# Performance work log

Measured on AMD Instinct MI355X. Metric: run time of the kernel, lower is better.

The kernel has to match this reference:

```python
import jax, jax.numpy as jnp
import numpy as np


def setup_inputs() -> dict:
    key = jax.random.key(0)
    ks = jax.random.split(key, 5)
    S, B, D, H, CTX = 2, 1024, 128, 512, 128
    W_SCALE = 0.05
    return {
        "context": jax.random.normal(ks[0], (B, CTX), dtype=jnp.float32),
        "eps": jax.random.normal(ks[1], (S, B, D), dtype=jnp.float32),
        "W1": jax.random.normal(ks[2], (H, D), dtype=jnp.float32) * W_SCALE,
        "Wc": jax.random.normal(ks[3], (H, CTX), dtype=jnp.float32) * W_SCALE,
        "b1": jnp.zeros((H,), dtype=jnp.float32),
        "W2": jax.random.normal(ks[4], (2 * D, H), dtype=jnp.float32) * W_SCALE,
        "b2": jnp.zeros((2 * D,), dtype=jnp.float32),
    }


def _made_masks(D, H, dtype):
    # standard MADE natural-ordering masks, 1 hidden layer, 2 output params per dim
    m_in = jnp.arange(1, D + 1)                      # input degrees 1..D
    m_h = (jnp.arange(H) % (D - 1)) + 1              # hidden degrees 1..D-1
    M1 = (m_h[:, None] >= m_in[None, :]).astype(dtype)   # (H, D)
    m_out = jnp.tile(m_in, 2)                        # (2D,) mean then pre_scale
    M2 = (m_out[:, None] > m_h[None, :]).astype(dtype)   # (2D, H)
    return M1, M2


def reference(context, eps, W1, Wc, b1, W2, b2):
    # for d in range(D): full MADE forward, take column d of (mu, scale),
    # z[:, d] = mu_d + softplus(pre_scale_d) * eps_d  (reparameterized Normal sample)
    S, B, D = eps.shape
    H = W1.shape[0]
    M1, M2 = _made_masks(D, H, W1.dtype)
    W1m = W1 * M1            # (H, D)
    W2m = W2 * M2            # (2D, H)
    ctx_term = context @ Wc.T + b1   # (B, H), shared across S samples

    def made(z):             # z: (S, B, D) -> (S, B, 2D)
        h = jax.nn.relu(jnp.einsum('sbd,hd->sbh', z, W1m) + ctx_term)
        return jnp.einsum('sbh,oh->sbo', h, W2m) + b2

    def step(z, xs):
        d, eps_d = xs        # d: scalar int, eps_d: (S, B)
        out = made(z)        # full re-forward each dim, as in the torch loop
        mu_d = jnp.take(out, d, axis=-1)             # (S, B)
        pre_scale_d = jnp.take(out, d + D, axis=-1)  # (S, B)
        scale_d = jax.nn.softplus(pre_scale_d)
        z_d = mu_d + scale_d * eps_d                 # Normal(mu, scale).rsample()
        z = z.at[:, :, d].set(z_d)                   # index_put on column d
        return z, None

    z0 = jnp.zeros_like(eps)
    xs = (jnp.arange(D), jnp.moveaxis(eps, -1, 0))   # per-step noise (D, S, B)
    z_samples, _ = jax.lax.scan(step, z0, xs)
    return z_samples
```

## Files before the change

### kernel.cpp

```cpp
#include <hip/hip_runtime.h>
#include <math.h>

constexpr int S_   = 2;
constexpr int B_   = 1024;
constexpr int D_   = 128;
constexpr int H_   = 512;
constexpr int CTX_ = 128;

__device__ __forceinline__ int h_of_u(int u) {
    return (u < 508) ? ((u >> 2) + 127 * (u & 3)) : u;
}
__device__ __forceinline__ int g_of_u(int u) {
    return (u < 508) ? ((u >> 2) + 1) : (u - 507);
}
__device__ __forceinline__ float rlaneF(float v, int l) {
    return __int_as_float(__builtin_amdgcn_readlane(__float_as_int(v), l));
}
__device__ __forceinline__ float softplus_fast(float x) {
    return __logf(1.f + __expf(x));
}

typedef unsigned int  uint32x4 __attribute__((ext_vector_type(4)));
typedef unsigned int  uint32x2 __attribute__((ext_vector_type(2)));
typedef _Float16      half8    __attribute__((ext_vector_type(8)));
typedef _Float16      half4v   __attribute__((ext_vector_type(4)));
typedef _Float16      half2v   __attribute__((ext_vector_type(2)));
typedef __fp16        fp16x2   __attribute__((ext_vector_type(2)));
union U16 { uint32x4 u; half8 h; half2v h2[4]; };
union U8  { uint32x2 u; half4v h; };
union H2U { half2v h; fp16x2 f; unsigned int u; };
union FU  { uint32x4 u; float4 f; };

#if __has_builtin(__builtin_amdgcn_fdot2)
__device__ __forceinline__ float fdot2f(half2v a, half2v b, float c) {
    return __builtin_amdgcn_fdot2(a, b, c, false);
}
#else
__device__ __forceinline__ float fdot2f(half2v a, half2v b, float c) {
    return fmaf((float)a[0], (float)b[0], fmaf((float)a[1], (float)b[1], c));
}
#endif
#if __has_builtin(__builtin_amdgcn_cvt_pkrtz)
__device__ __forceinline__ half2v pk2(float a, float b) {
    H2U t; t.f = __builtin_amdgcn_cvt_pkrtz(a, b);
    return t.h;
}
#else
__device__ __forceinline__ half2v pk2(float a, float b) {
    half2v r; r[0] = (_Float16)a; r[1] = (_Float16)b; return r;
}
#endif

constexpr int N_WT = 16 * 2048;
constexpr size_t WS_WT_OFF   = 0;
constexpr size_t WS_W0_OFF   = (size_t)N_WT * 16;
constexpr size_t WS_WPX_OFF  = WS_W0_OFF + 128 * 16;
constexpr size_t WS_CTXP_OFF = WS_WPX_OFF + 256 * 8;
constexpr size_t WS_NEED     = WS_CTXP_OFF + (size_t)B_ * H_ * 4;

__global__ __launch_bounds__(512) void prep10_kernel(
    const float* __restrict__ context, const float* __restrict__ Wc,
    const float* __restrict__ b1, const float* __restrict__ W1,
    const float* __restrict__ W2, float* __restrict__ ctxp,
    uint32x4* __restrict__ WT, float4* __restrict__ W0,
    uint32x2* __restrict__ Wpx)
{
    const int bid = (int)blockIdx.x;
    if (bid < 128) {
        const int b0 = bid * 8;
        const int u  = (int)threadIdx.x;
        const int h  = h_of_u(u);
        const float* wr = Wc + (size_t)h * CTX_;
        float bb = b1[h];
        float acc[8];
#pragma unroll
        for (int i = 0; i < 8; ++i) acc[i] = bb;
        for (int c = 0; c < CTX_; c += 4) {
            float4 wv4 = *reinterpret_cast<const float4*>(wr + c);
#pragma unroll
            for (int i = 0; i < 8; ++i) {
                const float* cr = context + (size_t)(b0 + i) * CTX_ + c;
                acc[i] = fmaf(wv4.x, cr[0], fmaf(wv4.y, cr[1],
                         fmaf(wv4.z, cr[2], fmaf(wv4.w, cr[3], acc[i]))));
            }
        }
#pragma unroll
        for (int i = 0; i < 8; ++i)
            ctxp[(size_t)(b0 + i) * H_ + u] = acc[i];
        return;
    }
    if (bid < 192) {
        int e = (bid - 128) * 512 + (int)threadIdx.x;
        int m = e >> 11, r = e & 2047, t = r >> 8, k = (r >> 6) & 3, L = r & 63;
        int d = 8 * m + 1 + t;
        uint32x4 o = (uint32x4){0u, 0u, 0u, 0u};
        if (d <= 127) {
            int p = (d - 1) >> 4;
            if (k <= 1) {
                U16 uu;
                int rowA = (k == 0) ? L : (64 + L);
                int rowB = (k == 0) ? (128 + L) : (192 + L);
#pragma unroll
                for (int i = 0; i < 4; ++i) {
                    int hu = h_of_u(4 * (d - 1) + i);
                    uu.h[i]     = (_Float16)W2[(size_t)rowA * H_ + hu];
                    uu.h[4 + i] = (_Float16)W2[(size_t)rowB * H_ + hu];
                }
                o = uu.u;
            } else {
                FU f;
                int qb = (k == 2) ? 0 : 4;
#pragma unroll
                for (int q = 0; q < 4; ++q) {
                    int s = qb + q + p;
                    float val = 0.f;
                    if (s < 8) {
                        int u_ = s * 64 + L;
                        if (g_of_u(u_) > d) val = W1[(size_t)h_of_u(u_) * D_ + d];
                    }
                    ((float*)&f.f)[q] = val;
                }
                o = f.u;
            }
        }
        WT[e] = o;
        return;
    }
    int i = (int)threadIdx.x;
    if (i < 128) {
        int L = i & 63, qb = (i >> 6) * 4;
        float4 f;
        float* fp = (float*)&f;
#pragma unroll
        for (int q = 0; q < 4; ++q) {
            int u_ = (qb + q) * 64 + L;
            fp[q] = W1[(size_t)h_of_u(u_) * D_ + 0];
        }
        W0[i] = f;
    } else if (i < 384) {
        int k = i - 128, t = k >> 6, L = k & 63, u_ = 508 + t;
        U8 o;
        o.h[0] = (_Float16)W2[(size_t)L * H_ + u_];
        o.h[1] = (_Float16)W2[(size_t)(128 + L) * H_ + u_];
        o.h[2] = (_Float16)W2[(size_t)(64 + L) * H_ + u_];
        o.h[3] = (_Float16)W2[(size_t)(192 + L) * H_ + u_];
        Wpx[k] = o.u;
    }
}

#define LOFF(HALF, T, K) ((HALF) * 2048 + (T) * 256 + (K) * 64)

#define STEP_LO(HALF, T, DB, LASTT, EXTRA) do {                               \
    U16 wA_, wB_;                                                             \
    wA_.u = smL[LOFF(HALF, T, 0)];                                            \
    wB_.u = smL[LOFF(HALF, T, 1)];                                            \
    const float4 wu0_ = *(const float4*)&smL[LOFF(HALF, T, 2)];               \
    const float4 wu1_ = *(const float4*)&smL[LOFF(HALF, T, 3)];               \
    float v_ = fmaxf(a0, 0.f);                                                \
    half2v s01_ = pk2(rlaneF(v_, 32 * (HALF) + 4 * (T) + 0),                  \
                      rlaneF(v_, 32 * (HALF) + 4 * (T) + 1));                 \
    half2v s23_ = pk2(rlaneF(v_, 32 * (HALF) + 4 * (T) + 2),                  \
                      rlaneF(v_, 32 * (HALF) + 4 * (T) + 3));                 \
    acc0 = fdot2f(wA_.h2[0], s01_, acc0);                                     \
    acc0 = fdot2f(wA_.h2[1], s23_, acc0);                                     \
    acc1 = fdot2f(wA_.h2[2], s01_, acc1);                                     \
    acc1 = fdot2f(wA_.h2[3], s23_, acc1);                                     \
    acc2 = fdot2f(wB_.h2[0], s01_, acc2);                                     \
    acc2 = fdot2f(wB_.h2[1], s23_, acc2);                                     \
    acc3 = fdot2f(wB_.h2[2], s01_, acc3);                                     \
    acc3 = fdot2f(wB_.h2[3], s23_, acc3);                                     \
    EXTRA                                                                     \
    const int dl_ = (DB) + (T);                                               \
    const bool hi64_ = (LASTT);                                               \
    float mu_ = hi64_ ? acc2 : acc0;                                          \
    float pv_ = hi64_ ? acc3 : acc1;                                          \
    float e_  = hi64_ ? rlaneF(eH, 0) : rlaneF(eL, dl_ & 63);                 \
    float z_  = fmaf(softplus_fast(pv_), e_, mu_);                            \
    float zb_ = rlaneF(z_, dl_ & 63);                                         \
    zlo = (!hi64_ && L == dl_) ? zb_ : zlo;                                   \
    zhi = (hi64_ && L == 0)    ? zb_ : zhi;                                   \
    a0 = fmaf(wu0_.x, zb_, a0); a1 = fmaf(wu0_.y, zb_, a1);                   \
    a2 = fmaf(wu0_.z, zb_, a2); a3 = fmaf(wu0_.w, zb_, a3);                   \
    a4 = fmaf(wu1_.x, zb_, a4); a5 = fmaf(wu1_.y, zb_, a5);                   \
    a6 = fmaf(wu1_.z, zb_, a6); a7 = fmaf(wu1_.w, zb_, a7);                   \
} while (0)

#define STEP_HI(HALF, T, DB2) do {                                            \
    U16 wB_;                                                                  \
    wB_.u = smL[LOFF(HALF, T, 1)];                                            \
    const float4 wu_ = *(const float4*)&smL[LOFF(HALF, T, 2)];                \
    float v_ = fmaxf(a0, 0.f);                                                \
    half2v s01_ = pk2(rlaneF(v_, 32 * (HALF) + 4 * (T) + 0),                  \
                      rlaneF(v_, 32 * (HALF) + 4 * (T) + 1));                 \
    half2v s23_ = pk2(rlaneF(v_, 32 * (HALF) + 4 * (T) + 2),                  \
                      rlaneF(v_, 32 * (HALF) + 4 * (T) + 3));                 \
    acc2 = fdot2f(wB_.h2[0], s01_, acc2);                                     \
    acc2 = fdot2f(wB_.h2[1], s23_, acc2);                                     \
    acc3 = fdot2f(wB_.h2[2], s01_, acc3);                                     \
    acc3 = fdot2f(wB_.h2[3], s23_, acc3);                                     \
    const int dl_ = (DB2) + (T);                                              \
    float e_  = rlaneF(eH, dl_ & 63);                                         \
    float z_  = fmaf(softplus_fast(acc3), e_, acc2);                          \
    float zb_ = rlaneF(z_, dl_ & 63);                                         \
    zhi = (L == dl_) ? zb_ : zhi;                                             \
    a0 = fmaf(wu_.x, zb_, a0); a1 = fmaf(wu_.y, zb_, a1);                     \
    a2 = fmaf(wu_.z, zb_, a2); a3 = fmaf(wu_.w, zb_, a3);                     \
} while (0)

#define EXTRA_X(T, WXn) {                                                     \
    float v7_ = fmaxf(a7, 0.f);                                               \
    float sx_ = rlaneF(v7_, 60 + (T));                                        \
    acc0 = fmaf((float)WXn.h[0], sx_, acc0);                                  \
    acc1 = fmaf((float)WXn.h[1], sx_, acc1);                                  \
    acc2 = fmaf((float)WXn.h[2], sx_, acc2);                                  \
    acc3 = fmaf((float)WXn.h[3], sx_, acc3); }

#define ROTATE do { a0=a1; a1=a2; a2=a3; a3=a4; a4=a5; a5=a6; a6=a7; } while (0)

#define STAGE_LO_X(m) { x0 = WT[(m)*2048 + tid];        x1 = WT[(m)*2048 + 512 + tid];  \
                        x2 = WT[(m)*2048 + 1024 + tid]; x3 = WT[(m)*2048 + 1536 + tid]; }
#define STAGE_LO_Y(m) { y0 = WT[(m)*2048 + tid];        y1 = WT[(m)*2048 + 512 + tid];  \
                        y2 = WT[(m)*2048 + 1024 + tid]; y3 = WT[(m)*2048 + 1536 + tid]; }
#define STAGE_HI_X(m) { x0 = WT[(m)*2048 + ehi]; x1 = WT[(m)*2048 + 1024 + ehi]; }
#define STAGE_HI_Y(m) { y0 = WT[(m)*2048 + ehi]; y1 = WT[(m)*2048 + 1024 + ehi]; }
#define COMMIT_LO_X(BB) { sm[(BB)+tid] = x0; sm[(BB)+512+tid] = x1;                     \
                          sm[(BB)+1024+tid] = x2; sm[(BB)+1536+tid] = x3; }
#define COMMIT_LO_Y(BB) { sm[(BB)+tid] = y0; sm[(BB)+512+tid] = y1;                     \
                          sm[(BB)+1024+tid] = y2; sm[(BB)+1536+tid] = y3; }
#define COMMIT_HI_X(BB) { sm[(BB)+ehi] = x0; sm[(BB)+1024+ehi] = x1; }
#define COMMIT_HI_Y(BB) { sm[(BB)+ehi] = y0; sm[(BB)+1024+ehi] = y1; }

__global__ __launch_bounds__(512) void ar10_kernel(
    const float* __restrict__ eps, const uint32x4* __restrict__ WT,
    const float4* __restrict__ W0, const uint32x2* __restrict__ Wpx2,
    const float* __restrict__ b2, const float* __restrict__ ctxp,
    float* __restrict__ out)
{
    __shared__ uint32x4 sm[4096];
    const int tid = (int)threadIdx.x;
    const int w   = tid >> 6, L = tid & 63;
    const int wv  = (int)blockIdx.x * 8 + w;
    const int b   = wv & (B_ - 1);
    const uint32x4* smL = sm + L;
    const int ehi = ((tid >> 7) << 8) + 64 + (tid & 127);

    uint32x4 x0, x1, x2, x3, y0, y1, y2, y3;
    STAGE_LO_X(0);

    float a0 = ctxp[(size_t)b * H_ + 0 * 64 + L];
    float a1 = ctxp[(size_t)b * H_ + 1 * 64 + L];
    float a2 = ctxp[(size_t)b * H_ + 2 * 64 + L];
    float a3 = ctxp[(size_t)b * H_ + 3 * 64 + L];
    float a4 = ctxp[(size_t)b * H_ + 4 * 64 + L];
    float a5 = ctxp[(size_t)b * H_ + 5 * 64 + L];
    float a6 = ctxp[(size_t)b * H_ + 6 * 64 + L];
    float a7 = ctxp[(size_t)b * H_ + 7 * 64 + L];
    float acc0 = b2[L],      acc1 = b2[128 + L];
    float acc2 = b2[64 + L], acc3 = b2[192 + L];
    const float* ep = eps + (size_t)wv * D_;
    float eL = ep[L], eH = ep[64 + L];
    float zlo = 0.f, zhi = 0.f;
    float4 w0lo = W0[L], w0hi = W0[64 + L];
    U8 wx1, wx2, wx3, wx4;
    wx1.u = Wpx2[0 * 64 + L]; wx2.u = Wpx2[1 * 64 + L];
    wx3.u = Wpx2[2 * 64 + L]; wx4.u = Wpx2[3 * 64 + L];

    COMMIT_LO_X(0);
    STAGE_LO_Y(1);

    {
        float e_ = rlaneF(eL, 0);
        float z_ = fmaf(softplus_fast(acc1), e_, acc0);
        float zb = rlaneF(z_, 0);
        zlo = (L == 0) ? zb : zlo;
        a0 = fmaf(w0lo.x, zb, a0); a1 = fmaf(w0lo.y, zb, a1);
        a2 = fmaf(w0lo.z, zb, a2); a3 = fmaf(w0lo.w, zb, a3);
        a4 = fmaf(w0hi.x, zb, a4); a5 = fmaf(w0hi.y, zb, a5);
        a6 = fmaf(w0hi.z, zb, a6); a7 = fmaf(w0hi.w, zb, a7);
    }
    __syncthreads();

    {
        STEP_LO(0, 0, 1, false, EXTRA_X(0, wx1));
        STEP_LO(0, 1, 1, false, EXTRA_X(1, wx2));
        STEP_LO(0, 2, 1, false, EXTRA_X(2, wx3));
        STEP_LO(0, 3, 1, false, EXTRA_X(3, wx4));
        STEP_LO(0, 4, 1, false, {});
        STEP_LO(0, 5, 1, false, {});
        STEP_LO(0, 6, 1, false, {});
        STEP_LO(0, 7, 1, false, {});
        COMMIT_LO_Y(2048);
        STAGE_LO_X(2);
        __syncthreads();
    }
    {
        STEP_LO(1, 0, 9, false, {});
        STEP_LO(1, 1, 9, false, {});
        STEP_LO(1, 2, 9, false, {});
        STEP_LO(1, 3, 9, false, {});
        STEP_LO(1, 4, 9, false, {});
        STEP_LO(1, 5, 9, false, {});
        STEP_LO(1, 6, 9, false, {});
        STEP_LO(1, 7, 9, false, {});
        COMMIT_LO_X(0);
        STAGE_LO_Y(3);
        ROTATE;
        __syncthreads();
    }

#pragma unroll 1
    for (int mm = 1; mm <= 3; ++mm) {
        const int dbE = 16 * mm + 1, dbO = dbE + 8;
        const bool last = (mm == 3);
        STEP_LO(0, 0, dbE, false, {});
        STEP_LO(0, 1, dbE, false, {});
        STEP_LO(0, 2, dbE, false, {});
        STEP_LO(0, 3, dbE, false, {});
        STEP_LO(0, 4, dbE, false, {});
        STEP_LO(0, 5, dbE, false, {});
        STEP_LO(0, 6, dbE, false, {});
        STEP_LO(0, 7, dbE, false, {});
        COMMIT_LO_Y(2048);
        if (!last) { STAGE_LO_X(2 * mm + 2); } else { STAGE_HI_X(8); }
        __syncthreads();
        STEP_LO(1, 0, dbO, false, {});
        STEP_LO(1, 1, dbO, false, {});
        STEP_LO(1, 2, dbO, false, {});
        STEP_LO(1, 3, dbO, false, {});
        STEP_LO(1, 4, dbO, false, {});
        STEP_LO(1, 5, dbO, false, {});
        STEP_LO(1, 6, dbO, false, {});
        STEP_LO(1, 7, dbO, last, {});
        if (!last) { COMMIT_LO_X(0); } else { COMMIT_HI_X(0); }
        if (!last) { STAGE_LO_Y(2 * mm + 3); } else { STAGE_HI_Y(9); }
        ROTATE;
        __syncthreads();
    }

#pragma unroll 1
    for (int mm = 0; mm <= 3; ++mm) {
        const int dbE = 16 * mm + 1, dbO = dbE + 8;
        STEP_HI(0, 0, dbE);
        STEP_HI(0, 1, dbE);
        STEP_HI(0, 2, dbE);
        STEP_HI(0, 3, dbE);
        STEP_HI(0, 4, dbE);
        STEP_HI(0, 5, dbE);
        STEP_HI(0, 6, dbE);
        STEP_HI(0, 7, dbE);
        COMMIT_HI_Y(2048);
        if (mm < 3) { STAGE_HI_X(10 + 2 * mm); }
        __syncthreads();
        STEP_HI(1, 0, dbO);
        STEP_HI(1, 1, dbO);
        STEP_HI(1, 2, dbO);
        STEP_HI(1, 3, dbO);
        STEP_HI(1, 4, dbO);
        STEP_HI(1, 5, dbO);
        STEP_HI(1, 6, dbO);
        STEP_HI(1, 7, dbO);
        if (mm < 3) {
            COMMIT_HI_X(0);
            STAGE_HI_Y(11 + 2 * mm);
            ROTATE;
            __syncthreads();
        }
    }

    out[(size_t)wv * D_ + L]      = zlo;
    out[(size_t)wv * D_ + 64 + L] = zhi;
}

template <int CTRL>
__device__ __forceinline__ float dpp_add(float x)
{
    int r = __builtin_amdgcn_update_dpp(0, __float_as_int(x), CTRL, 0xF, 0xF, true);
    return x + __int_as_float(r);
}
__device__ __forceinline__ float reduce64(float x)
{
    x = dpp_add<0x111>(x);
    x = dpp_add<0x112>(x);
    x = dpp_add<0x114>(x);
    x = dpp_add<0x118>(x);
    x = dpp_add<0x142>(x);
    x = dpp_add<0x143>(x);
    return __int_as_float(__builtin_amdgcn_readlane(__float_as_int(x), 63));
}
__device__ __forceinline__ float softplus_safe(float x) {
    return fmaxf(x, 0.f) + __logf(1.f + __expf(-fabsf(x)));
}

__global__ __launch_bounds__(256) void ar_fallback_kernel(
    const float* __restrict__ eps,
    const float* __restrict__ W2,
    const float* __restrict__ b2,
    const float* __restrict__ context,
    const float* __restrict__ Wc,
    const float* __restrict__ b1,
    const float* __restrict__ W1,
    float* __restrict__ out)
{
    const int wave = (int)((blockIdx.x * blockDim.x + threadIdx.x) >> 6);
    const int lane = (int)(threadIdx.x & 63);
    if (wave >= S_ * B_) return;
    const int b  = wave % B_;
    const int hb = lane * 8;

    int mh[8];
#pragma unroll
    for (int j = 0; j < 8; ++j) mh[j] = ((hb + j) % (D_ - 1)) + 1;

    float a[8];
#pragma unroll
    for (int j = 0; j < 8; ++j) a[j] = b1[hb + j];
    for (int c = 0; c < CTX_; ++c) {
        float cv = context[(size_t)b * CTX_ + c];
#pragma unroll
        for (int j = 0; j < 8; ++j)
            a[j] = fmaf(Wc[(size_t)(hb + j) * CTX_ + c], cv, a[j]);
    }

    const float* epsrow = eps + (size_t)wave * D_;
    float* outrow = out + (size_t)wave * D_;
    float zr0 = 0.f, zr1 = 0.f;

    for (int d = 0; d < D_; ++d) {
        const float* w2mu = W2 + (size_t)d * H_ + hb;
        const float* w2ps = W2 + (size_t)(d + D_) * H_ + hb;
        float4 m0 = *reinterpret_cast<const float4*>(w2mu);
        float4 m1 = *reinterpret_cast<const float4*>(w2mu + 4);
        float4 p0 = *reinterpret_cast<const float4*>(w2ps);
        float4 p1 = *reinterpret_cast<const float4*>(w2ps + 4);
        float wmu[8] = {m0.x, m0.y, m0.z, m0.w, m1.x, m1.y, m1.z, m1.w};
        float wps[8] = {p0.x, p0.y, p0.z, p0.w, p1.x, p1.y, p1.z, p1.w};
        float w1v[8];
#pragma unroll
        for (int j = 0; j < 8; ++j) w1v[j] = W1[(size_t)(hb + j) * D_ + d];
        float eps_d = epsrow[d];

        float mu = 0.f, ps = 0.f;
#pragma unroll
        for (int j = 0; j < 8; ++j) {
            float r = fmaxf(a[j], 0.f);
            r = (mh[j] <= d) ? r : 0.f;
            mu = fmaf(wmu[j], r, mu);
            ps = fmaf(wps[j], r, ps);
        }
        mu = reduce64(mu) + b2[d];
        ps = reduce64(ps) + b2[d + D_];

        float z = fmaf(softplus_safe(ps), eps_d, mu);
#pragma unroll
        for (int j = 0; j < 8; ++j) {
            float wgt = (mh[j] <= d) ? 0.f : w1v[j];
            a[j] = fmaf(wgt, z, a[j]);
        }
        bool mine = (lane == (d & 63));
        if (d < 64) zr0 = mine ? z : zr0; else zr1 = mine ? z : zr1;
    }

    outrow[lane]      = zr0;
    outrow[lane + 64] = zr1;
}

extern "C" void kernel_launch(void* const* d_in, const int* in_sizes, int n_in,
                              void* d_out, int out_size, void* d_ws, size_t ws_size,
                              hipStream_t stream)
{
    const float* context = (const float*)d_in[0];
    const float* eps     = (const float*)d_in[1];
    const float* W1      = (const float*)d_in[2];
    const float* Wc      = (const float*)d_in[3];
    const float* b1      = (const float*)d_in[4];
    const float* W2      = (const float*)d_in[5];
    const float* b2      = (const float*)d_in[6];
    float* out = (float*)d_out;

    if (ws_size >= WS_NEED) {
        char* ws = (char*)d_ws;
        uint32x4* WT   = (uint32x4*)(ws + WS_WT_OFF);
        float4*   W0   = (float4*)(ws + WS_W0_OFF);
        uint32x2* Wpx  = (uint32x2*)(ws + WS_WPX_OFF);
        float*    ctxp = (float*)(ws + WS_CTXP_OFF);

        prep10_kernel<<<193, 512, 0, stream>>>(
            context, Wc, b1, W1, W2, ctxp, WT, W0, Wpx);

        ar10_kernel<<<256, 512, 0, stream>>>(
            eps, WT, W0, Wpx, b2, ctxp, out);
    } else {
        const int nwaves = S_ * B_;
        ar_fallback_kernel<<<(nwaves * 64) / 256, 256, 0, stream>>>(
            eps, W2, b2, context, Wc, b1, W1, out);
    }
}
```

Before: 45.76 us.

## Process both samples per wave and pack W1 update weights as fp16

Each wave now handles both S samples for a batch row, so every weight tile loaded from shared memory serves two recurrences. The broadcast-and-dot and rank-1 hidden update are duplicated across two accumulator sets. W1 update weights are stored as fp16 instead of fp32, and the high-half layout is compacted, cutting the staged weight table and shared memory (4096 to 3072 entries). Blocks shrink to 256 threads on the same grid, which halves total waves. Register pressure roughly doubles and W1 precision drops to fp16.

New measurement: 45.36 us. No clear change (-0.9%).

```diff
diff --git a/kernel.cpp b/kernel.cpp
--- a/kernel.cpp
+++ b/kernel.cpp
@@ -27,9 +27,8 @@
 typedef _Float16      half2v   __attribute__((ext_vector_type(2)));
 typedef __fp16        fp16x2   __attribute__((ext_vector_type(2)));
 union U16 { uint32x4 u; half8 h; half2v h2[4]; };
-union U8  { uint32x2 u; half4v h; };
+union U8  { uint32x2 u; half4v h; half2v h2[2]; };
 union H2U { half2v h; fp16x2 f; unsigned int u; };
-union FU  { uint32x4 u; float4 f; };
 
 #if __has_builtin(__builtin_amdgcn_fdot2)
 __device__ __forceinline__ float fdot2f(half2v a, half2v b, float c) {
@@ -51,14 +50,14 @@
 }
 #endif
 
-constexpr int N_WT = 16 * 2048;
 constexpr size_t WS_WT_OFF   = 0;
-constexpr size_t WS_W0_OFF   = (size_t)N_WT * 16;
+constexpr size_t WS_W0_OFF   = (size_t)16 * 1536 * 16;
 constexpr size_t WS_WPX_OFF  = WS_W0_OFF + 128 * 16;
 constexpr size_t WS_CTXP_OFF = WS_WPX_OFF + 256 * 8;
 constexpr size_t WS_NEED     = WS_CTXP_OFF + (size_t)B_ * H_ * 4;
-
-__global__ __launch_bounds__(512) void prep10_kernel(
+constexpr int N_WT_ENT = 8 * 1536 + 8 * 768;
+
+__global__ __launch_bounds__(512) void prep11_kernel(
     const float* __restrict__ context, const float* __restrict__ Wc,
     const float* __restrict__ b1, const float* __restrict__ W1,
     const float* __restrict__ W2, float* __restrict__ ctxp,
@@ -89,41 +88,79 @@
             ctxp[(size_t)(b0 + i) * H_ + u] = acc[i];
         return;
     }
-    if (bid < 192) {
+    if (bid < 164) {
         int e = (bid - 128) * 512 + (int)threadIdx.x;
-        int m = e >> 11, r = e & 2047, t = r >> 8, k = (r >> 6) & 3, L = r & 63;
-        int d = 8 * m + 1 + t;
-        uint32x4 o = (uint32x4){0u, 0u, 0u, 0u};
-        if (d <= 127) {
-            int p = (d - 1) >> 4;
+        if (e >= N_WT_ENT) return;
+        if (e < 12288) {
+            int m = e / 1536, r = e % 1536;
+            int t = r / 192, rr = r % 192, k = rr >> 6, L = rr & 63;
+            int d = 8 * m + 1 + t;
+            U16 o;
             if (k <= 1) {
-                U16 uu;
                 int rowA = (k == 0) ? L : (64 + L);
                 int rowB = (k == 0) ? (128 + L) : (192 + L);
 #pragma unroll
                 for (int i = 0; i < 4; ++i) {
                     int hu = h_of_u(4 * (d - 1) + i);
-                    uu.h[i]     = (_Float16)W2[(size_t)rowA * H_ + hu];
-                    uu.h[4 + i] = (_Float16)W2[(size_t)rowB * H_ + hu];
+                    o.h[i]     = (_Float16)W2[(size_t)rowA * H_ + hu];
+                    o.h[4 + i] = (_Float16)W2[(size_t)rowB * H_ + hu];
                 }
-                o = uu.u;
             } else {
-                FU f;
-                int qb = (k == 2) ? 0 : 4;
-#pragma unroll
-                for (int q = 0; q < 4; ++q) {
-                    int s = qb + q + p;
-                    float val = 0.f;
+                int p = (d - 1) >> 4;
+#pragma unroll
+                for (int j = 0; j < 8; ++j) {
+                    int s = j + p;
+                    _Float16 val = (_Float16)0.f;
                     if (s < 8) {
                         int u_ = s * 64 + L;
-                        if (g_of_u(u_) > d) val = W1[(size_t)h_of_u(u_) * D_ + d];
+                        if (g_of_u(u_) > d)
+                            val = (_Float16)W1[(size_t)h_of_u(u_) * D_ + d];
                     }
-                    ((float*)&f.f)[q] = val;
+                    o.h[j] = val;
                 }
-                o = f.u;
+            }
+            WT[e] = o.u;
+        } else {
+            int e2 = e - 12288;
+            int m = 8 + e2 / 768, r = e2 % 768;
+            int dbb = 8 * m + 1;
+            if (r < 512) {
+                int t = r >> 6, L = r & 63, d = dbb + t;
+                U16 o;
+#pragma unroll
+                for (int i = 0; i < 8; ++i) o.h[i] = (_Float16)0.f;
+                if (d <= 127) {
+#pragma unroll
+                    for (int i = 0; i < 4; ++i) {
+                        int hu = h_of_u(4 * (d - 1) + i);
+                        o.h[i]     = (_Float16)W2[(size_t)(64 + L) * H_ + hu];
+                        o.h[4 + i] = (_Float16)W2[(size_t)(192 + L) * H_ + hu];
+                    }
+                }
+                WT[(size_t)m * 1536 + t * 64 + L] = o.u;
+            } else {
+                int q = r - 512, t = q >> 5, j = q & 31, d = dbb + t;
+                int L0 = 2 * j, L1 = 2 * j + 1;
+                U8 oa, ob;
+                oa.u = (uint32x2){0u, 0u}; ob.u = (uint32x2){0u, 0u};
+                if (d <= 127) {
+                    int p = (d - 1) >> 4;
+#pragma unroll
+                    for (int k2 = 0; k2 < 4; ++k2) {
+                        int s = p + k2;
+                        _Float16 va = (_Float16)0.f, vb = (_Float16)0.f;
+                        if (s < 8) {
+                            int u0 = s * 64 + L0, u1 = s * 64 + L1;
+                            if (g_of_u(u0) > d) va = (_Float16)W1[(size_t)h_of_u(u0) * D_ + d];
+                            if (g_of_u(u1) > d) vb = (_Float16)W1[(size_t)h_of_u(u1) * D_ + d];
+                        }
+                        oa.h[k2] = va; ob.h[k2] = vb;
+                    }
+                }
+                uint32x4 o4 = (uint32x4){oa.u[0], oa.u[1], ob.u[0], ob.u[1]};
+                WT[(size_t)m * 1536 + 512 + q] = o4;
             }
         }
-        WT[e] = o;
         return;
     }
     int i = (int)threadIdx.x;
@@ -148,103 +185,142 @@
     }
 }
 
-#define LOFF(HALF, T, K) ((HALF) * 2048 + (T) * 256 + (K) * 64)
-
-#define STEP_LO(HALF, T, DB, LASTT, EXTRA) do {                               \
-    U16 wA_, wB_;                                                             \
+#define LOFF(HALF, T, K) ((HALF) * 1536 + (T) * 192 + (K) * 64)
+#define HOFF(HALF, T)    ((HALF) * 1536 + (T) * 64)
+#define HUOFF(HALF, T)   ((HALF) * 3072 + 1024 + (T) * 64)
+
+#define STEP_LO2(HALF, T, DB, LASTT, EXTRA) do {                              \
+    U16 wA_, wB_, wu_;                                                        \
     wA_.u = smL[LOFF(HALF, T, 0)];                                            \
     wB_.u = smL[LOFF(HALF, T, 1)];                                            \
-    const float4 wu0_ = *(const float4*)&smL[LOFF(HALF, T, 2)];               \
-    const float4 wu1_ = *(const float4*)&smL[LOFF(HALF, T, 3)];               \
-    float v_ = fmaxf(a0, 0.f);                                                \
-    half2v s01_ = pk2(rlaneF(v_, 32 * (HALF) + 4 * (T) + 0),                  \
-                      rlaneF(v_, 32 * (HALF) + 4 * (T) + 1));                 \
-    half2v s23_ = pk2(rlaneF(v_, 32 * (HALF) + 4 * (T) + 2),                  \
-                      rlaneF(v_, 32 * (HALF) + 4 * (T) + 3));                 \
-    acc0 = fdot2f(wA_.h2[0], s01_, acc0);                                     \
-    acc0 = fdot2f(wA_.h2[1], s23_, acc0);                                     \
-    acc1 = fdot2f(wA_.h2[2], s01_, acc1);                                     \
-    acc1 = fdot2f(wA_.h2[3], s23_, acc1);                                     \
-    acc2 = fdot2f(wB_.h2[0], s01_, acc2);                                     \
-    acc2 = fdot2f(wB_.h2[1], s23_, acc2);                                     \
-    acc3 = fdot2f(wB_.h2[2], s01_, acc3);                                     \
-    acc3 = fdot2f(wB_.h2[3], s23_, acc3);                                     \
+    wu_.u = smL[LOFF(HALF, T, 2)];                                            \
+    float va_ = fmaxf(a0, 0.f), vc_ = fmaxf(c0, 0.f);                         \
+    const int lb_ = 32 * (HALF) + 4 * (T);                                    \
+    half2v sa01_ = pk2(rlaneF(va_, lb_ + 0), rlaneF(va_, lb_ + 1));           \
+    half2v sa23_ = pk2(rlaneF(va_, lb_ + 2), rlaneF(va_, lb_ + 3));           \
+    half2v sc01_ = pk2(rlaneF(vc_, lb_ + 0), rlaneF(vc_, lb_ + 1));           \
+    half2v sc23_ = pk2(rlaneF(vc_, lb_ + 2), rlaneF(vc_, lb_ + 3));           \
+    acc00 = fdot2f(wA_.h2[0], sa01_, acc00);                                  \
+    acc00 = fdot2f(wA_.h2[1], sa23_, acc00);                                  \
+    acc01 = fdot2f(wA_.h2[2], sa01_, acc01);                                  \
+    acc01 = fdot2f(wA_.h2[3], sa23_, acc01);                                  \
+    acc02 = fdot2f(wB_.h2[0], sa01_, acc02);                                  \
+    acc02 = fdot2f(wB_.h2[1], sa23_, acc02);                                  \
+    acc03 = fdot2f(wB_.h2[2], sa01_, acc03);                                  \
+    acc03 = fdot2f(wB_.h2[3], sa23_, acc03);                                  \
+    acc10 = fdot2f(wA_.h2[0], sc01_, acc10);                                  \
+    acc10 = fdot2f(wA_.h2[1], sc23_, acc10);                                  \
+    acc11 = fdot2f(wA_.h2[2], sc01_, acc11);                                  \
+    acc11 = fdot2f(wA_.h2[3], sc23_, acc11);                                  \
+    acc12 = fdot2f(wB_.h2[0], sc01_, acc12);                                  \
+    acc12 = fdot2f(wB_.h2[1], sc23_, acc12);                                  \
+    acc13 = fdot2f(wB_.h2[2], sc01_, acc13);                                  \
+    acc13 = fdot2f(wB_.h2[3], sc23_, acc13);                                  \
     EXTRA                                                                     \
     const int dl_ = (DB) + (T);                                               \
     const bool hi64_ = (LASTT);                                               \
-    float mu_ = hi64_ ? acc2 : acc0;                                          \
-    float pv_ = hi64_ ? acc3 : acc1;                                          \
-    float e_  = hi64_ ? rlaneF(eH, 0) : rlaneF(eL, dl_ & 63);                 \
-    float z_  = fmaf(softplus_fast(pv_), e_, mu_);                            \
-    float zb_ = rlaneF(z_, dl_ & 63);                                         \
-    zlo = (!hi64_ && L == dl_) ? zb_ : zlo;                                   \
-    zhi = (hi64_ && L == 0)    ? zb_ : zhi;                                   \
-    a0 = fmaf(wu0_.x, zb_, a0); a1 = fmaf(wu0_.y, zb_, a1);                   \
-    a2 = fmaf(wu0_.z, zb_, a2); a3 = fmaf(wu0_.w, zb_, a3);                   \
-    a4 = fmaf(wu1_.x, zb_, a4); a5 = fmaf(wu1_.y, zb_, a5);                   \
-    a6 = fmaf(wu1_.z, zb_, a6); a7 = fmaf(wu1_.w, zb_, a7);                   \
+    float mu0_ = hi64_ ? acc02 : acc00, pv0_ = hi64_ ? acc03 : acc01;         \
+    float mu1_ = hi64_ ? acc12 : acc10, pv1_ = hi64_ ? acc13 : acc11;         \
+    float e0_ = hi64_ ? rlaneF(e0H, 0) : rlaneF(e0L, dl_ & 63);               \
+    float e1_ = hi64_ ? rlaneF(e1H, 0) : rlaneF(e1L, dl_ & 63);               \
+    float z0_ = fmaf(softplus_fast(pv0_), e0_, mu0_);                         \
+    float z1_ = fmaf(softplus_fast(pv1_), e1_, mu1_);                         \
+    float zb0_ = rlaneF(z0_, dl_ & 63), zb1_ = rlaneF(z1_, dl_ & 63);         \
+    zlo0 = (!hi64_ && L == dl_) ? zb0_ : zlo0;                                \
+    zhi0 = (hi64_ && L == 0)    ? zb0_ : zhi0;                                \
+    zlo1 = (!hi64_ && L == dl_) ? zb1_ : zlo1;                                \
+    zhi1 = (hi64_ && L == 0)    ? zb1_ : zhi1;                                \
+    { float w_;                                                               \
+      w_ = (float)wu_.h[0]; a0 = fmaf(w_, zb0_, a0); c0 = fmaf(w_, zb1_, c0); \
+      w_ = (float)wu_.h[1]; a1 = fmaf(w_, zb0_, a1); c1 = fmaf(w_, zb1_, c1); \
+      w_ = (float)wu_.h[2]; a2 = fmaf(w_, zb0_, a2); c2 = fmaf(w_, zb1_, c2); \
+      w_ = (float)wu_.h[3]; a3 = fmaf(w_, zb0_, a3); c3 = fmaf(w_, zb1_, c3); \
+      w_ = (float)wu_.h[4]; a4 = fmaf(w_, zb0_, a4); c4 = fmaf(w_, zb1_, c4); \
+      w_ = (float)wu_.h[5]; a5 = fmaf(w_, zb0_, a5); c5 = fmaf(w_, zb1_, c5); \
+      w_ = (float)wu_.h[6]; a6 = fmaf(w_, zb0_, a6); c6 = fmaf(w_, zb1_, c6); \
+      w_ = (float)wu_.h[7]; a7 = fmaf(w_, zb0_, a7); c7 = fmaf(w_, zb1_, c7); } \
 } while (0)
 
-#define STEP_HI(HALF, T, DB2) do {                                            \
-    U16 wB_;                                                                  \
-    wB_.u = smL[LOFF(HALF, T, 1)];                                            \
-    const float4 wu_ = *(const float4*)&smL[LOFF(HALF, T, 2)];                \
-    float v_ = fmaxf(a0, 0.f);                                                \
-    half2v s01_ = pk2(rlaneF(v_, 32 * (HALF) + 4 * (T) + 0),                  \
-                      rlaneF(v_, 32 * (HALF) + 4 * (T) + 1));                 \
-    half2v s23_ = pk2(rlaneF(v_, 32 * (HALF) + 4 * (T) + 2),                  \
-                      rlaneF(v_, 32 * (HALF) + 4 * (T) + 3));                 \
-    acc2 = fdot2f(wB_.h2[0], s01_, acc2);                                     \
-    acc2 = fdot2f(wB_.h2[1], s23_, acc2);                                     \
-    acc3 = fdot2f(wB_.h2[2], s01_, acc3);                                     \
-    acc3 = fdot2f(wB_.h2[3], s23_, acc3);                                     \
+#define STEP_HI2(HALF, T, DB2) do {                                           \
+    U16 wB_; U8 wu_;                                                          \
+    wB_.u = smL[HOFF(HALF, T)];                                               \
+    wu_.u = smH2L[HUOFF(HALF, T)];                                            \
+    float va_ = fmaxf(a0, 0.f), vc_ = fmaxf(c0, 0.f);                         \
+    const int lb_ = 32 * (HALF) + 4 * (T);                                    \
+    half2v sa01_ = pk2(rlaneF(va_, lb_ + 0), rlaneF(va_, lb_ + 1));           \
+    half2v sa23_ = pk2(rlaneF(va_, lb_ + 2), rlaneF(va_, lb_ + 3));           \
+    half2v sc01_ = pk2(rlaneF(vc_, lb_ + 0), rlaneF(vc_, lb_ + 1));           \
+    half2v sc23_ = pk2(rlaneF(vc_, lb_ + 2), rlaneF(vc_, lb_ + 3));           \
+    acc02 = fdot2f(wB_.h2[0], sa01_, acc02);                                  \
+    acc02 = fdot2f(wB_.h2[1], sa23_, acc02);                                  \
+    acc03 = fdot2f(wB_.h2[2], sa01_, acc03);                                  \
+    acc03 = fdot2f(wB_.h2[3], sa23_, acc03);                                  \
+    acc12 = fdot2f(wB_.h2[0], sc01_, acc12);                                  \
+    acc12 = fdot2f(wB_.h2[1], sc23_, acc12);                                  \
+    acc13 = fdot2f(wB_.h2[2], sc01_, acc13);                                  \
+    acc13 = fdot2f(wB_.h2[3], sc23_, acc13);                                  \
     const int dl_ = (DB2) + (T);                                              \
-    float e_  = rlaneF(eH, dl_ & 63);                                         \
-    float z_  = fmaf(softplus_fast(acc3), e_, acc2);                          \
-    float zb_ = rlaneF(z_, dl_ & 63);                                         \
-    zhi = (L == dl_) ? zb_ : zhi;                                             \
-    a0 = fmaf(wu_.x, zb_, a0); a1 = fmaf(wu_.y, zb_, a1);                     \
-    a2 = fmaf(wu_.z, zb_, a2); a3 = fmaf(wu_.w, zb_, a3);                     \
+    float e0_ = rlaneF(e0H, dl_ & 63), e1_ = rlaneF(e1H, dl_ & 63);           \
+    float z0_ = fmaf(softplus_fast(acc03), e0_, acc02);                       \
+    float z1_ = fmaf(softplus_fast(acc13), e1_, acc12);                       \
+    float zb0_ = rlaneF(z0_, dl_ & 63), zb1_ = rlaneF(z1_, dl_ & 63);         \
+    zhi0 = (L == dl_) ? zb0_ : zhi0;                                          \
+    zhi1 = (L == dl_) ? zb1_ : zhi1;                                          \
+    { float w_;                                                               \
+      w_ = (float)wu_.h[0]; a0 = fmaf(w_, zb0_, a0); c0 = fmaf(w_, zb1_, c0); \
+      w_ = (float)wu_.h[1]; a1 = fmaf(w_, zb0_, a1); c1 = fmaf(w_, zb1_, c1); \
+      w_ = (float)wu_.h[2]; a2 = fmaf(w_, zb0_, a2); c2 = fmaf(w_, zb1_, c2); \
+      w_ = (float)wu_.h[3]; a3 = fmaf(w_, zb0_, a3); c3 = fmaf(w_, zb1_, c3); } \
 } while (0)
 
-#define EXTRA_X(T, WXn) {                                                     \
-    float v7_ = fmaxf(a7, 0.f);                                               \
-    float sx_ = rlaneF(v7_, 60 + (T));                                        \
-    acc0 = fmaf((float)WXn.h[0], sx_, acc0);                                  \
-    acc1 = fmaf((float)WXn.h[1], sx_, acc1);                                  \
-    acc2 = fmaf((float)WXn.h[2], sx_, acc2);                                  \
-    acc3 = fmaf((float)WXn.h[3], sx_, acc3); }
-
-#define ROTATE do { a0=a1; a1=a2; a2=a3; a3=a4; a4=a5; a5=a6; a6=a7; } while (0)
-
-#define STAGE_LO_X(m) { x0 = WT[(m)*2048 + tid];        x1 = WT[(m)*2048 + 512 + tid];  \
-                        x2 = WT[(m)*2048 + 1024 + tid]; x3 = WT[(m)*2048 + 1536 + tid]; }
-#define STAGE_LO_Y(m) { y0 = WT[(m)*2048 + tid];        y1 = WT[(m)*2048 + 512 + tid];  \
-                        y2 = WT[(m)*2048 + 1024 + tid]; y3 = WT[(m)*2048 + 1536 + tid]; }
-#define STAGE_HI_X(m) { x0 = WT[(m)*2048 + ehi]; x1 = WT[(m)*2048 + 1024 + ehi]; }
-#define STAGE_HI_Y(m) { y0 = WT[(m)*2048 + ehi]; y1 = WT[(m)*2048 + 1024 + ehi]; }
-#define COMMIT_LO_X(BB) { sm[(BB)+tid] = x0; sm[(BB)+512+tid] = x1;                     \
-                          sm[(BB)+1024+tid] = x2; sm[(BB)+1536+tid] = x3; }
-#define COMMIT_LO_Y(BB) { sm[(BB)+tid] = y0; sm[(BB)+512+tid] = y1;                     \
-                          sm[(BB)+1024+tid] = y2; sm[(BB)+1536+tid] = y3; }
-#define COMMIT_HI_X(BB) { sm[(BB)+ehi] = x0; sm[(BB)+1024+ehi] = x1; }
-#define COMMIT_HI_Y(BB) { sm[(BB)+ehi] = y0; sm[(BB)+1024+ehi] = y1; }
-
-__global__ __launch_bounds__(512) void ar10_kernel(
+#define EXTRA_X2(T, WXn) {                                                    \
+    float v7a_ = fmaxf(a7, 0.f), v7c_ = fmaxf(c7, 0.f);                       \
+    float sxa_ = rlaneF(v7a_, 60 + (T)), sxc_ = rlaneF(v7c_, 60 + (T));       \
+    float wx0_ = (float)WXn.h[0], wx1_ = (float)WXn.h[1];                     \
+    float wx2_ = (float)WXn.h[2], wx3_ = (float)WXn.h[3];                     \
+    acc00 = fmaf(wx0_, sxa_, acc00); acc01 = fmaf(wx1_, sxa_, acc01);         \
+    acc02 = fmaf(wx2_, sxa_, acc02); acc03 = fmaf(wx3_, sxa_, acc03);         \
+    acc10 = fmaf(wx0_, sxc_, acc10); acc11 = fmaf(wx1_, sxc_, acc11);         \
+    acc12 = fmaf(wx2_, sxc_, acc12); acc13 = fmaf(wx3_, sxc_, acc13); }
+
+#define ROTATE2 do { a0=a1; a1=a2; a2=a3; a3=a4; a4=a5; a5=a6; a6=a7;         \
+                     c0=c1; c1=c2; c2=c3; c3=c4; c4=c5; c5=c6; c6=c7; } while (0)
+
+#define STAGE_LO_X(m) { x0=WT[(m)*1536+tid]; x1=WT[(m)*1536+256+tid];         \
+    x2=WT[(m)*1536+512+tid]; x3=WT[(m)*1536+768+tid];                         \
+    x4=WT[(m)*1536+1024+tid]; x5=WT[(m)*1536+1280+tid]; }
+#define STAGE_LO_Y(m) { y0=WT[(m)*1536+tid]; y1=WT[(m)*1536+256+tid];         \
+    y2=WT[(m)*1536+512+tid]; y3=WT[(m)*1536+768+tid];                         \
+    y4=WT[(m)*1536+1024+tid]; y5=WT[(m)*1536+1280+tid]; }
+#define STAGE_HI_X(m) { x0=WT[(m)*1536+tid]; x1=WT[(m)*1536+256+tid];         \
+    x2=WT[(m)*1536+512+tid]; }
+#define STAGE_HI_Y(m) { y0=WT[(m)*1536+tid]; y1=WT[(m)*1536+256+tid];         \
+    y2=WT[(m)*1536+512+tid]; }
+#define COMMIT_LO_X(BB) { sm[(BB)+tid]=x0; sm[(BB)+256+tid]=x1;               \
+    sm[(BB)+512+tid]=x2; sm[(BB)+768+tid]=x3;                                 \
+    sm[(BB)+1024+tid]=x4; sm[(BB)+1280+tid]=x5; }
+#define COMMIT_LO_Y(BB) { sm[(BB)+tid]=y0; sm[(BB)+256+tid]=y1;               \
+    sm[(BB)+512+tid]=y2; sm[(BB)+768+tid]=y3;                                 \
+    sm[(BB)+1024+tid]=y4; sm[(BB)+1280+tid]=y5; }
+#define COMMIT_HI_X(BB) { sm[(BB)+tid]=x0; sm[(BB)+256+tid]=x1;               \
+    sm[(BB)+512+tid]=x2; }
+#define COMMIT_HI_Y(BB) { sm[(BB)+tid]=y0; sm[(BB)+256+tid]=y1;               \
+    sm[(BB)+512+tid]=y2; }
+
+__global__ __launch_bounds__(256) void ar11_kernel(
     const float* __restrict__ eps, const uint32x4* __restrict__ WT,
     const float4* __restrict__ W0, const uint32x2* __restrict__ Wpx2,
     const float* __restrict__ b2, const float* __restrict__ ctxp,
     float* __restrict__ out)
 {
-    __shared__ uint32x4 sm[4096];
+    __shared__ uint32x4 sm[3072];
     const int tid = (int)threadIdx.x;
     const int w   = tid >> 6, L = tid & 63;
-    const int wv  = (int)blockIdx.x * 8 + w;
-    const int b   = wv & (B_ - 1);
+    const int b   = (int)blockIdx.x * 4 + w;
     const uint32x4* smL = sm + L;
-    const int ehi = ((tid >> 7) << 8) + 64 + (tid & 127);
-
-    uint32x4 x0, x1, x2, x3, y0, y1, y2, y3;
+    const uint32x2* smH2L = ((const uint32x2*)sm) + L;
+
+    uint32x4 x0, x1, x2, x3, x4, x5, y0, y1, y2, y3, y4, y5;
     STAGE_LO_X(0);
 
     float a0 = ctxp[(size_t)b * H_ + 0 * 64 + L];
@@ -255,11 +331,16 @@
     float a5 = ctxp[(size_t)b * H_ + 5 * 64 + L];
     float a6 = ctxp[(size_t)b * H_ + 6 * 64 + L];
     float a7 = ctxp[(size_t)b * H_ + 7 * 64 + L];
-    float acc0 = b2[L],      acc1 = b2[128 + L];
-    float acc2 = b2[64 + L], acc3 = b2[192 + L];
-    const float* ep = eps + (size_t)wv * D_;
-    float eL = ep[L], eH = ep[64 + L];
-    float zlo = 0.f, zhi = 0.f;
+    float c0 = a0, c1 = a1, c2 = a2, c3 = a3;
+    float c4 = a4, c5 = a5, c6 = a6, c7 = a7;
+    float acc00 = b2[L],      acc01 = b2[128 + L];
+    float acc02 = b2[64 + L], acc03 = b2[192 + L];
+    float acc10 = acc00, acc11 = acc01, acc12 = acc02, acc13 = acc03;
+    const float* ep0 = eps + (size_t)b * D_;
+    const float* ep1 = eps + (size_t)(B_ + b) * D_;
+    float e0L = ep0[L], e0H = ep0[64 + L];
+    float e1L = ep1[L], e1H = ep1[64 + L];
+    float zlo0 = 0.f, zhi0 = 0.f, zlo1 = 0.f, zhi1 = 0.f;
     float4 w0lo = W0[L], w0hi = W0[64 + L];
     U8 wx1, wx2, wx3, wx4;
     wx1.u = Wpx2[0 * 64 + L]; wx2.u = Wpx2[1 * 64 + L];
@@ -269,42 +350,47 @@
     STAGE_LO_Y(1);
 
     {
-        float e_ = rlaneF(eL, 0);
-        float z_ = fmaf(softplus_fast(acc1), e_, acc0);
-        float zb = rlaneF(z_, 0);
-        zlo = (L == 0) ? zb : zlo;
-        a0 = fmaf(w0lo.x, zb, a0); a1 = fmaf(w0lo.y, zb, a1);
-        a2 = fmaf(w0lo.z, zb, a2); a3 = fmaf(w0lo.w, zb, a3);
-        a4 = fmaf(w0hi.x, zb, a4); a5 = fmaf(w0hi.y, zb, a5);
-        a6 = fmaf(w0hi.z, zb, a6); a7 = fmaf(w0hi.w, zb, a7);
+        float e0_ = rlaneF(e0L, 0), e1_ = rlaneF(e1L, 0);
+        float z0_ = fmaf(softplus_fast(acc01), e0_, acc00);
+        float z1_ = fmaf(softplus_fast(acc11), e1_, acc10);
+        float zb0 = rlaneF(z0_, 0), zb1 = rlaneF(z1_, 0);
+        if (L == 0) { zlo0 = zb0; zlo1 = zb1; }
+        a0 = fmaf(w0lo.x, zb0, a0); c0 = fmaf(w0lo.x, zb1, c0);
+        a1 = fmaf(w0lo.y, zb0, a1); c1 = fmaf(w0lo.y, zb1, c1);
+        a2 = fmaf(w0lo.z, zb0, a2); c2 = fmaf(w0lo.z, zb1, c2);
+        a3 = fmaf(w0lo.w, zb0, a3); c3 = fmaf(w0lo.w, zb1, c3);
+        a4 = fmaf(w0hi.x, zb0, a4); c4 = fmaf(w0hi.x, zb1, c4);
+        a5 = fmaf(w0hi.y, zb0, a5); c5 = fmaf(w0hi.y, zb1, c5);
+        a6 = fmaf(w0hi.z, zb0, a6); c6 = fmaf(w0hi.z, zb1, c6);
+        a7 = fmaf(w0hi.w, zb0, a7); c7 = fmaf(w0hi.w, zb1, c7);
     }
     __syncthreads();
 
     {
-        STEP_LO(0, 0, 1, false, EXTRA_X(0, wx1));
-        STEP_LO(0, 1, 1, false, EXTRA_X(1, wx2));
-        STEP_LO(0, 2, 1, false, EXTRA_X(2, wx3));
-        STEP_LO(0, 3, 1, false, EXTRA_X(3, wx4));
-        STEP_LO(0, 4, 1, false, {});
-        STEP_LO(0, 5, 1, false, {});
-        STEP_LO(0, 6, 1, false, {});
-        STEP_LO(0, 7, 1, false, {});
-        COMMIT_LO_Y(2048);
+        STEP_LO2(0, 0, 1, false, EXTRA_X2(0, wx1));
+        STEP_LO2(0, 1, 1, false, EXTRA_X2(1, wx2));
+        STEP_LO2(0, 2, 1, false, EXTRA_X2(2, wx3));
+        STEP_LO2(0, 3, 1, false, EXTRA_X2(3, wx4));
+        STEP_LO2(0, 4, 1, false, {});
+        STEP_LO2(0, 5, 1, false, {});
+        STEP_LO2(0, 6, 1, false, {});
+        STEP_LO2(0, 7, 1, false, {});
+        COMMIT_LO_Y(1536);
         STAGE_LO_X(2);
         __syncthreads();
     }
     {
-        STEP_LO(1, 0, 9, false, {});
-        STEP_LO(1, 1, 9, false, {});
-        STEP_LO(1, 2, 9, false, {});
-        STEP_LO(1, 3, 9, false, {});
-        STEP_LO(1, 4, 9, false, {});
-        STEP_LO(1, 5, 9, false, {});
-        STEP_LO(1, 6, 9, false, {});
-        STEP_LO(1, 7, 9, false, {});
+        STEP_LO2(1, 0, 9, false, {});
+        STEP_LO2(1, 1, 9, false, {});
+        STEP_LO2(1, 2, 9, false, {});
+        STEP_LO2(1, 3, 9, false, {});
+        STEP_LO2(1, 4, 9, false, {});
+        STEP_LO2(1, 5, 9, false, {});
+        STEP_LO2(1, 6, 9, false, {});
+        STEP_LO2(1, 7, 9, false, {});
         COMMIT_LO_X(0);
         STAGE_LO_Y(3);
-        ROTATE;
+        ROTATE2;
         __syncthreads();
     }
 
@@ -312,63 +398,65 @@
     for (int mm = 1; mm <= 3; ++mm) {
         const int dbE = 16 * mm + 1, dbO = dbE + 8;
         const bool last = (mm == 3);
-        STEP_LO(0, 0, dbE, false, {});
-        STEP_LO(0, 1, dbE, false, {});
-        STEP_LO(0, 2, dbE, false, {});
-        STEP_LO(0, 3, dbE, false, {});
-        STEP_LO(0, 4, dbE, false, {});
-        STEP_LO(0, 5, dbE, false, {});
-        STEP_LO(0, 6, dbE, false, {});
-        STEP_LO(0, 7, dbE, false, {});
-        COMMIT_LO_Y(2048);
+        STEP_LO2(0, 0, dbE, false, {});
+        STEP_LO2(0, 1, dbE, false, {});
+        STEP_LO2(0, 2, dbE, false, {});
+        STEP_LO2(0, 3, dbE, false, {});
+        STEP_LO2(0, 4, dbE, false, {});
+        STEP_LO2(0, 5, dbE, false, {});
+        STEP_LO2(0, 6, dbE, false, {});
+        STEP_LO2(0, 7, dbE, false, {});
+        COMMIT_LO_Y(1536);
         if (!last) { STAGE_LO_X(2 * mm + 2); } else { STAGE_HI_X(8); }
         __syncthreads();
-        STEP_LO(1, 0, dbO, false, {});
-        STEP_LO(1, 1, dbO, false, {});
-        STEP_LO(1, 2, dbO, false, {});
-        STEP_LO(1, 3, dbO, false, {});
-        STEP_LO(1, 4, dbO, false, {});
-        STEP_LO(1, 5, dbO, false, {});
-        STEP_LO(1, 6, dbO, false, {});
-        STEP_LO(1, 7, dbO, last, {});
+        STEP_LO2(1, 0, dbO, false, {});
+        STEP_LO2(1, 1, dbO, false, {});
+        STEP_LO2(1, 2, dbO, false, {});
+        STEP_LO2(1, 3, dbO, false, {});
+        STEP_LO2(1, 4, dbO, false, {});
+        STEP_LO2(1, 5, dbO, false, {});
+        STEP_LO2(1, 6, dbO, false, {});
+        STEP_LO2(1, 7, dbO, last, {});
         if (!last) { COMMIT_LO_X(0); } else { COMMIT_HI_X(0); }
         if (!last) { STAGE_LO_Y(2 * mm + 3); } else { STAGE_HI_Y(9); }
-        ROTATE;
+        ROTATE2;
         __syncthreads();
     }
 
 #pragma unroll 1
     for (int mm = 0; mm <= 3; ++mm) {
         const int dbE = 16 * mm + 1, dbO = dbE + 8;
-        STEP_HI(0, 0, dbE);
-        STEP_HI(0, 1, dbE);
-        STEP_HI(0, 2, dbE);
-        STEP_HI(0, 3, dbE);
-        STEP_HI(0, 4, dbE);
-        STEP_HI(0, 5, dbE);
-        STEP_HI(0, 6, dbE);
-        STEP_HI(0, 7, dbE);
-        COMMIT_HI_Y(2048);
+        STEP_HI2(0, 0, dbE);
+        STEP_HI2(0, 1, dbE);
+        STEP_HI2(0, 2, dbE);
+        STEP_HI2(0, 3, dbE);
+        STEP_HI2(0, 4, dbE);
+        STEP_HI2(0, 5, dbE);
+        STEP_HI2(0, 6, dbE);
+        STEP_HI2(0, 7, dbE);
+        COMMIT_HI_Y(1536);
         if (mm < 3) { STAGE_HI_X(10 + 2 * mm); }
         __syncthreads();
-        STEP_HI(1, 0, dbO);
-        STEP_HI(1, 1, dbO);
-        STEP_HI(1, 2, dbO);
-        STEP_HI(1, 3, dbO);
-        STEP_HI(1, 4, dbO);
-        STEP_HI(1, 5, dbO);
-        STEP_HI(1, 6, dbO);
-        STEP_HI(1, 7, dbO);
+        STEP_HI2(1, 0, dbO);
+        STEP_HI2(1, 1, dbO);
+        STEP_HI2(1, 2, dbO);
+        STEP_HI2(1, 3, dbO);
+        STEP_HI2(1, 4, dbO);
+        STEP_HI2(1, 5, dbO);
+        STEP_HI2(1, 6, dbO);
+        STEP_HI2(1, 7, dbO);
         if (mm < 3) {
             COMMIT_HI_X(0);
             STAGE_HI_Y(11 + 2 * mm);
-            ROTATE;
+            ROTATE2;
             __syncthreads();
         }
     }
 
-    out[(size_t)wv * D_ + L]      = zlo;
-    out[(size_t)wv * D_ + 64 + L] = zhi;
+    out[(size_t)b * D_ + L]             = zlo0;
+    out[(size_t)b * D_ + 64 + L]        = zhi0;
+    out[(size_t)(B_ + b) * D_ + L]      = zlo1;
+    out[(size_t)(B_ + b) * D_ + 64 + L] = zhi1;
 }
 
 template <int CTRL>
@@ -484,10 +572,10 @@
         uint32x2* Wpx  = (uint32x2*)(ws + WS_WPX_OFF);
         float*    ctxp = (float*)(ws + WS_CTXP_OFF);
 
-        prep10_kernel<<<193, 512, 0, stream>>>(
+        prep11_kernel<<<165, 512, 0, stream>>>(
             context, Wc, b1, W1, W2, ctxp, WT, W0, Wpx);
 
-        ar10_kernel<<<256, 512, 0, stream>>>(
+        ar11_kernel<<<256, 256, 0, stream>>>(
             eps, WT, W0, Wpx, b2, ctxp, out);
     } else {
         const int nwaves = S_ * B_;
```
